# Kernel tuning notes

Measured on AMD Instinct MI355X. Metric: run time of the kernel, lower is better.

Reference implementation:

```python
import jax, jax.numpy as jnp
import numpy as np

NEG_INIT = -1.0e9


def setup_inputs() -> dict:
    key = jax.random.key(0)
    k1, k2, k3, k4, k5, k6, k7 = jax.random.split(key, 7)
    N, D, d_att, G = 262144, 512, 128, 512
    feats = jax.random.normal(k1, (N, D), dtype=jnp.float32)
    index = jnp.sort(jax.random.randint(k2, (N,), 0, G, dtype=jnp.int64))
    # torch Linear params: weight (out,in), bias (out,)
    Vw = jax.random.normal(k3, (d_att, D), dtype=jnp.float32) / np.sqrt(D)
    Vb = jax.random.normal(k4, (d_att,), dtype=jnp.float32) * 0.01
    Uw = jax.random.normal(k5, (d_att, D), dtype=jnp.float32) / np.sqrt(D)
    Ub = jax.random.normal(k6, (d_att,), dtype=jnp.float32) * 0.01
    ww = jax.random.normal(k7, (1, d_att), dtype=jnp.float32) / np.sqrt(d_att)
    return {"feats": feats, "index": index, "num_groups": G,
            "Vw": Vw, "Vb": Vb, "Uw": Uw, "Ub": Ub, "ww": ww}


def reference(feats, index, num_groups, Vw, Vb, Uw, Ub, ww):
    # gated attention MLP: A = tanh(V x) * sigmoid(U x); scores = w A
    A = jnp.tanh(feats @ Vw.T + Vb) * jax.nn.sigmoid(feats @ Uw.T + Ub)  # (N, d_att)
    scores = (A @ ww.T)[:, 0]  # (N,)
    # segment max with -1e9 init (matches scatter_reduce amax include_self)
    max_per_group = jax.ops.segment_max(scores, index, num_segments=num_groups)
    max_per_group = jnp.maximum(max_per_group, NEG_INIT)  # empty segments -> -1e9
    exp_scores = jnp.exp(scores - max_per_group[index])
    denom = jax.ops.segment_sum(exp_scores, index, num_segments=num_groups)
    weights = exp_scores / (denom[index] + 1e-8)
    # weighted scatter-sum pooling: (num_groups, D)
    out = jax.ops.segment_sum(feats * weights[:, None], index, num_segments=num_groups)
    return out
```

## Files before the change

kernel.cpp:

```cpp
#include <hip/hip_runtime.h>
#include <hip/hip_fp8.h>
#include <cstddef>

#define NEG_INIT -1.0e9f

typedef _Float16 f16x8 __attribute__((ext_vector_type(8)));
typedef _Float16 f16x4 __attribute__((ext_vector_type(4)));
typedef float f32x4 __attribute__((ext_vector_type(4)));

constexpr int D   = 512;
constexpr int BM  = 32;
constexpr int BK  = 32;
constexpr int NKS = D / BK;
constexpr int LDH = 520;
constexpr int LDR = 528;
constexpr int PS  = 516;
constexpr float RSC  = 2048.f;
constexpr float RISC = 1.f / 2048.f;

__global__ __launch_bounds__(64) void k_wprep(const float* __restrict__ Vw,
                                              const float* __restrict__ Uw,
                                              _Float16* __restrict__ Wfrag) {
    const int bid  = blockIdx.x;
    const int lane = threadIdx.x;
    const int j    = bid & 3;
    const int ks   = (bid >> 2) & 15;
    const int wc   = bid >> 6;
    const int l15  = lane & 15;
    const int kgrp = lane >> 4;
    const float* src = (j < 2 ? Vw + (size_t)(wc * 32 + j * 16 + l15) * D
                              : Uw + (size_t)(wc * 32 + (j - 2) * 16 + l15) * D)
                       + ks * BK + kgrp * 8;
    f16x8 h;
    #pragma unroll
    for (int e = 0; e < 8; ++e) h[e] = (_Float16)src[e];
    *(f16x8*)(Wfrag + ((size_t)bid * 64 + lane) * 8) = h;
}

__global__ __launch_bounds__(256) void k_bounds(const int* __restrict__ index,
                                                int N, int G,
                                                int* __restrict__ start) {
    int g = blockIdx.x * blockDim.x + threadIdx.x;
    if (g > G) return;
    int lo = 0, hi = N;
    while (lo < hi) {
        int mid = (lo + hi) >> 1;
        if (index[mid] < g) lo = mid + 1; else hi = mid;
    }
    start[g] = lo;
}

__global__ __launch_bounds__(512, 6) void k_fused(
    const float* __restrict__ feats, const _Float16* __restrict__ Wfrag,
    const float* __restrict__ Vb, const float* __restrict__ Ub,
    const float* __restrict__ ww, const int* __restrict__ index,
    const int* __restrict__ start, float* __restrict__ P, int N)
{
    __shared__ __align__(16) _Float16 Xh[BM][LDH];
    __shared__ __align__(4)  unsigned char Xr8[BM * LDR];
    __shared__ float sred[8][BM];
    __shared__ float srow[BM];
    __shared__ float evals[BM];

    const int t    = threadIdx.x;
    const int lane = t & 63;
    const int wc   = t >> 6;
    const int l15  = lane & 15;
    const int kgrp = lane >> 4;
    const int blk  = blockIdx.x;
    const int rb   = blk * BM;

    {
        const int xrow = t >> 4;
        const int xcb  = t & 15;
        const float* xg = feats + (size_t)min(rb + xrow, N - 1) * D + xcb * 4;
        #pragma unroll
        for (int k = 0; k < 8; ++k) {
            f32x4 v = *(const f32x4*)(xg + k * 64);
            f16x4 h;
            unsigned int rp = 0;
            #pragma unroll
            for (int e = 0; e < 4; ++e) {
                h[e] = (_Float16)v[e];
                float res = (v[e] - (float)h[e]) * RSC;
                __hip_fp8_e4m3 q(res);
                rp |= (unsigned int)q.__x << (8 * e);
            }
            *(f16x4*)&Xh[xrow][k * 64 + xcb * 4] = h;
            *(unsigned int*)&Xr8[xrow * LDR + k * 64 + xcb * 4] = rp;
        }
    }
    __syncthreads();

    const _Float16* wbV = Wfrag + (size_t)(wc >> 1) * 32768
                                + (size_t)(wc & 1) * 512 + (size_t)lane * 8;
    const _Float16* wbU = wbV + 1024;

    f32x4 accV[2], accU[2];
    #pragma unroll
    for (int i = 0; i < 2; ++i) {
        accV[i] = (f32x4){0.f, 0.f, 0.f, 0.f};
        accU[i] = (f32x4){0.f, 0.f, 0.f, 0.f};
    }

    #pragma unroll 4
    for (int ks = 0; ks < NKS; ++ks) {
        f16x8 bv = *(const f16x8*)(wbV + (size_t)ks * 2048);
        f16x8 bu = *(const f16x8*)(wbU + (size_t)ks * 2048);
        f16x8 ha[2];
        #pragma unroll
        for (int i = 0; i < 2; ++i)
            ha[i] = *(const f16x8*)&Xh[i * 16 + l15][ks * BK + kgrp * 8];
        #pragma unroll
        for (int i = 0; i < 2; ++i) {
            accV[i] = __builtin_amdgcn_mfma_f32_16x16x32_f16(ha[i], bv, accV[i], 0, 0, 0);
            accU[i] = __builtin_amdgcn_mfma_f32_16x16x32_f16(ha[i], bu, accU[i], 0, 0, 0);
        }
    }

    {
        const int c = wc * 16 + l15;
        const float vb = Vb[c], ub = Ub[c], w = ww[c];
        float part[2][4];
        #pragma unroll
        for (int i = 0; i < 2; ++i)
            #pragma unroll
            for (int r = 0; r < 4; ++r) {
                float v = accV[i][r] + vb;
                float u = accU[i][r] + ub;
                part[i][r] = w * tanhf(v) * (1.f / (1.f + expf(-u)));
            }
        #pragma unroll
        for (int off = 1; off < 16; off <<= 1)
            #pragma unroll
            for (int i = 0; i < 2; ++i)
                #pragma unroll
                for (int r = 0; r < 4; ++r)
                    part[i][r] += __shfl_xor(part[i][r], off);
        if (l15 == 0) {
            #pragma unroll
            for (int i = 0; i < 2; ++i)
                #pragma unroll
                for (int r = 0; r < 4; ++r)
                    sred[wc][i * 16 + kgrp * 4 + r] = part[i][r];
        }
    }
    __syncthreads();
    if (t < BM) {
        float s = sred[0][t];
        #pragma unroll
        for (int w8 = 1; w8 < 8; ++w8) s += sred[w8][t];
        srow[t] = s;
    }
    __syncthreads();

    const int gl = index[rb];
    const int gh = index[rb + BM - 1];
    for (int g = gl + wc; g <= gh; g += 8) {
        const int r0 = max(start[g], rb), r1 = min(start[g + 1], rb + BM);
        if (r1 <= r0) continue;
        const bool in = (lane >= r0 - rb) && (lane < r1 - rb);
        float m = in ? srow[lane] : NEG_INIT;
        #pragma unroll
        for (int off = 32; off; off >>= 1) m = fmaxf(m, __shfl_xor(m, off));
        float e = in ? expf(srow[lane] - m) : 0.f;
        if (in) evals[lane] = e;
        float s = e;
        #pragma unroll
        for (int off = 32; off; off >>= 1) s += __shfl_xor(s, off);
        if (lane == 0) {
            float* slot = P + (size_t)(blk + g) * PS;
            slot[0] = m; slot[1] = s;
        }
    }
    __syncthreads();

    for (int g = gl; g <= gh; ++g) {
        const int r0 = max(start[g], rb), r1 = min(start[g + 1], rb + BM);
        if (r1 <= r0) continue;
        float a = 0.f;
        for (int r = r0; r < r1; ++r) {
            const int rr = r - rb;
            float h = (float)Xh[rr][t];
            __hip_fp8_e4m3 q;
            q.__x = Xr8[rr * LDR + t];
            float x = fmaf((float)q, RISC, h);
            a = fmaf(evals[rr], x, a);
        }
        P[(size_t)(blk + g) * PS + 4 + t] = a;
    }
}

__global__ __launch_bounds__(512) void k_merge(const float* __restrict__ P,
                                               const int* __restrict__ start,
                                               float* __restrict__ out)
{
    const int g = blockIdx.x, t = threadIdx.x;
    const int s0 = start[g], s1 = start[g + 1];
    if (s0 >= s1) { out[(size_t)g * D + t] = 0.f; return; }
    const int b0 = s0 >> 5, b1 = (s1 - 1) >> 5;
    float M = NEG_INIT;
    for (int b = b0; b <= b1; ++b)
        M = fmaxf(M, P[(size_t)(b + g) * PS]);
    float den = 0.f, acc = 0.f;
    for (int b = b0; b <= b1; ++b) {
        const float* slot = P + (size_t)(b + g) * PS;
        float w = expf(slot[0] - M);
        den += w * slot[1];
        acc += w * slot[4 + t];
    }
    out[(size_t)g * D + t] = acc / (den + 1e-8f);
}

extern "C" void kernel_launch(void* const* d_in, const int* in_sizes, int n_in,
                              void* d_out, int out_size, void* d_ws, size_t ws_size,
                              hipStream_t stream) {
    const float* feats = (const float*)d_in[0];
    const int*   index = (const int*)d_in[1];
    const float* Vw = (const float*)d_in[3];
    const float* Vb = (const float*)d_in[4];
    const float* Uw = (const float*)d_in[5];
    const float* Ub = (const float*)d_in[6];
    const float* ww = (const float*)d_in[7];
    float* out = (float*)d_out;

    const int N = in_sizes[1];
    const int G = out_size / D;
    const int nblk = (N + BM - 1) / BM;

    _Float16* Wfrag = (_Float16*)d_ws;
    int* start      = (int*)(Wfrag + (size_t)256 * 512);
    size_t off      = (size_t)256 * 512 * 2 + (G + 1) * 4;
    off             = (off + 15) & ~(size_t)15;
    float* P        = (float*)((char*)d_ws + off);

    hipLaunchKernelGGL(k_wprep, dim3(256), dim3(64), 0, stream, Vw, Uw, Wfrag);
    hipLaunchKernelGGL(k_bounds, dim3((G + 1 + 255) / 256), dim3(256), 0, stream,
                       index, N, G, start);
    hipLaunchKernelGGL(k_fused, dim3(nblk), dim3(512), 0, stream,
                       feats, Wfrag, Vb, Ub, ww, index, start, P, N);
    hipLaunchKernelGGL(k_merge, dim3(G), dim3(512), 0, stream, P, start, out);
}
```

Baseline: 239.3 us.

## Make fused kernel persistent over tiles with register-prefetched feature loads

Each block now processes 16 consecutive 32-row tiles instead of one, prefetching the next tile's feature rows into registers while the current tile's MFMA, softmax and pooling run. The aim is to hide global-load latency behind compute and amortize block setup. This cuts the grid size 16x and holds 32 extra float registers per thread, so the occupancy hint drops from 6 to 4. It also adds a barrier per tile.

```diff
diff --git a/kernel.cpp b/kernel.cpp
--- a/kernel.cpp
+++ b/kernel.cpp
@@ -12,6 +12,7 @@
 constexpr int BM  = 32;
 constexpr int BK  = 32;
 constexpr int NKS = D / BK;
+constexpr int TPB = 16;
 constexpr int LDH = 520;
 constexpr int LDR = 528;
 constexpr int PS  = 516;
@@ -50,7 +51,7 @@
     start[g] = lo;
 }
 
-__global__ __launch_bounds__(512, 6) void k_fused(
+__global__ __launch_bounds__(512, 4) void k_fused(
     const float* __restrict__ feats, const _Float16* __restrict__ Wfrag,
     const float* __restrict__ Vb, const float* __restrict__ Ub,
     const float* __restrict__ ww, const int* __restrict__ index,
@@ -67,127 +68,153 @@
     const int wc   = t >> 6;
     const int l15  = lane & 15;
     const int kgrp = lane >> 4;
-    const int blk  = blockIdx.x;
-    const int rb   = blk * BM;
-
-    {
-        const int xrow = t >> 4;
-        const int xcb  = t & 15;
-        const float* xg = feats + (size_t)min(rb + xrow, N - 1) * D + xcb * 4;
+
+    const int nTiles    = (N + BM - 1) / BM;
+    const int tile_base = blockIdx.x * TPB;
+    const int tile_end  = min(tile_base + TPB, nTiles);
+    if (tile_base >= nTiles) return;
+
+    const int xrow = t >> 4;
+    const int xcb  = t & 15;
+
+    float4 xa[8];
+    auto issueX = [&](int tile) {
+        const float* xg = feats + (size_t)min(tile * BM + xrow, N - 1) * D + xcb * 4;
+        #pragma unroll
+        for (int k = 0; k < 8; ++k)
+            xa[k] = *(const float4*)(xg + k * 64);
+    };
+    auto commitX = [&]() {
         #pragma unroll
         for (int k = 0; k < 8; ++k) {
-            f32x4 v = *(const f32x4*)(xg + k * 64);
+            float4 v = xa[k];
             f16x4 h;
             unsigned int rp = 0;
             #pragma unroll
             for (int e = 0; e < 4; ++e) {
-                h[e] = (_Float16)v[e];
-                float res = (v[e] - (float)h[e]) * RSC;
+                float ve = (&v.x)[e];
+                h[e] = (_Float16)ve;
+                float res = (ve - (float)h[e]) * RSC;
                 __hip_fp8_e4m3 q(res);
                 rp |= (unsigned int)q.__x << (8 * e);
             }
             *(f16x4*)&Xh[xrow][k * 64 + xcb * 4] = h;
             *(unsigned int*)&Xr8[xrow * LDR + k * 64 + xcb * 4] = rp;
         }
-    }
-    __syncthreads();
+    };
 
     const _Float16* wbV = Wfrag + (size_t)(wc >> 1) * 32768
                                 + (size_t)(wc & 1) * 512 + (size_t)lane * 8;
     const _Float16* wbU = wbV + 1024;
 
-    f32x4 accV[2], accU[2];
-    #pragma unroll
-    for (int i = 0; i < 2; ++i) {
-        accV[i] = (f32x4){0.f, 0.f, 0.f, 0.f};
-        accU[i] = (f32x4){0.f, 0.f, 0.f, 0.f};
-    }
-
-    #pragma unroll 4
-    for (int ks = 0; ks < NKS; ++ks) {
-        f16x8 bv = *(const f16x8*)(wbV + (size_t)ks * 2048);
-        f16x8 bu = *(const f16x8*)(wbU + (size_t)ks * 2048);
-        f16x8 ha[2];
-        #pragma unroll
-        for (int i = 0; i < 2; ++i)
-            ha[i] = *(const f16x8*)&Xh[i * 16 + l15][ks * BK + kgrp * 8];
+    issueX(tile_base);
+    commitX();
+    if (tile_base + 1 < tile_end) issueX(tile_base + 1);
+    __syncthreads();
+
+    for (int it = 0; it < TPB && tile_base + it < nTiles; ++it) {
+        const int tile = tile_base + it;
+        const int rb   = tile * BM;
+
+        f32x4 accV[2], accU[2];
         #pragma unroll
         for (int i = 0; i < 2; ++i) {
-            accV[i] = __builtin_amdgcn_mfma_f32_16x16x32_f16(ha[i], bv, accV[i], 0, 0, 0);
-            accU[i] = __builtin_amdgcn_mfma_f32_16x16x32_f16(ha[i], bu, accU[i], 0, 0, 0);
-        }
-    }
-
-    {
-        const int c = wc * 16 + l15;
-        const float vb = Vb[c], ub = Ub[c], w = ww[c];
-        float part[2][4];
-        #pragma unroll
-        for (int i = 0; i < 2; ++i)
-            #pragma unroll
-            for (int r = 0; r < 4; ++r) {
-                float v = accV[i][r] + vb;
-                float u = accU[i][r] + ub;
-                part[i][r] = w * tanhf(v) * (1.f / (1.f + expf(-u)));
-            }
-        #pragma unroll
-        for (int off = 1; off < 16; off <<= 1)
+            accV[i] = (f32x4){0.f, 0.f, 0.f, 0.f};
+            accU[i] = (f32x4){0.f, 0.f, 0.f, 0.f};
+        }
+        #pragma unroll 4
+        for (int ks = 0; ks < NKS; ++ks) {
+            f16x8 bv = *(const f16x8*)(wbV + (size_t)ks * 2048);
+            f16x8 bu = *(const f16x8*)(wbU + (size_t)ks * 2048);
+            f16x8 ha[2];
+            #pragma unroll
+            for (int i = 0; i < 2; ++i)
+                ha[i] = *(const f16x8*)&Xh[i * 16 + l15][ks * BK + kgrp * 8];
+            #pragma unroll
+            for (int i = 0; i < 2; ++i) {
+                accV[i] = __builtin_amdgcn_mfma_f32_16x16x32_f16(ha[i], bv, accV[i], 0, 0, 0);
+                accU[i] = __builtin_amdgcn_mfma_f32_16x16x32_f16(ha[i], bu, accU[i], 0, 0, 0);
+            }
+        }
+
+        {
+            const int c = wc * 16 + l15;
+            const float vb = Vb[c], ub = Ub[c], w = ww[c];
+            float part[2][4];
             #pragma unroll
             for (int i = 0; i < 2; ++i)
                 #pragma unroll
-                for (int r = 0; r < 4; ++r)
-                    part[i][r] += __shfl_xor(part[i][r], off);
-        if (l15 == 0) {
-            #pragma unroll
-            for (int i = 0; i < 2; ++i)
+                for (int r = 0; r < 4; ++r) {
+                    float v = accV[i][r] + vb;
+                    float u = accU[i][r] + ub;
+                    part[i][r] = w * tanhf(v) * (1.f / (1.f + expf(-u)));
+                }
+            #pragma unroll
+            for (int off = 1; off < 16; off <<= 1)
                 #pragma unroll
-                for (int r = 0; r < 4; ++r)
-                    sred[wc][i * 16 + kgrp * 4 + r] = part[i][r];
-        }
-    }
-    __syncthreads();
-    if (t < BM) {
-        float s = sred[0][t];
-        #pragma unroll
-        for (int w8 = 1; w8 < 8; ++w8) s += sred[w8][t];
-        srow[t] = s;
-    }
-    __syncthreads();
-
-    const int gl = index[rb];
-    const int gh = index[rb + BM - 1];
-    for (int g = gl + wc; g <= gh; g += 8) {
-        const int r0 = max(start[g], rb), r1 = min(start[g + 1], rb + BM);
-        if (r1 <= r0) continue;
-        const bool in = (lane >= r0 - rb) && (lane < r1 - rb);
-        float m = in ? srow[lane] : NEG_INIT;
-        #pragma unroll
-        for (int off = 32; off; off >>= 1) m = fmaxf(m, __shfl_xor(m, off));
-        float e = in ? expf(srow[lane] - m) : 0.f;
-        if (in) evals[lane] = e;
-        float s = e;
-        #pragma unroll
-        for (int off = 32; off; off >>= 1) s += __shfl_xor(s, off);
-        if (lane == 0) {
-            float* slot = P + (size_t)(blk + g) * PS;
-            slot[0] = m; slot[1] = s;
-        }
-    }
-    __syncthreads();
-
-    for (int g = gl; g <= gh; ++g) {
-        const int r0 = max(start[g], rb), r1 = min(start[g + 1], rb + BM);
-        if (r1 <= r0) continue;
-        float a = 0.f;
-        for (int r = r0; r < r1; ++r) {
-            const int rr = r - rb;
-            float h = (float)Xh[rr][t];
-            __hip_fp8_e4m3 q;
-            q.__x = Xr8[rr * LDR + t];
-            float x = fmaf((float)q, RISC, h);
-            a = fmaf(evals[rr], x, a);
-        }
-        P[(size_t)(blk + g) * PS + 4 + t] = a;
+                for (int i = 0; i < 2; ++i)
+                    #pragma unroll
+                    for (int r = 0; r < 4; ++r)
+                        part[i][r] += __shfl_xor(part[i][r], off);
+            if (l15 == 0) {
+                #pragma unroll
+                for (int i = 0; i < 2; ++i)
+                    #pragma unroll
+                    for (int r = 0; r < 4; ++r)
+                        sred[wc][i * 16 + kgrp * 4 + r] = part[i][r];
+            }
+        }
+        __syncthreads();
+        if (t < BM) {
+            float s = sred[0][t];
+            #pragma unroll
+            for (int w8 = 1; w8 < 8; ++w8) s += sred[w8][t];
+            srow[t] = s;
+        }
+        __syncthreads();
+
+        const int gl = index[rb];
+        const int gh = index[min(rb + BM - 1, N - 1)];
+        for (int g = gl + wc; g <= gh; g += 8) {
+            const int r0 = max(start[g], rb), r1 = min(start[g + 1], rb + BM);
+            if (r1 <= r0) continue;
+            const bool in = (lane >= r0 - rb) && (lane < r1 - rb);
+            float m = in ? srow[lane] : NEG_INIT;
+            #pragma unroll
+            for (int off = 32; off; off >>= 1) m = fmaxf(m, __shfl_xor(m, off));
+            float e = in ? expf(srow[lane] - m) : 0.f;
+            if (in) evals[lane] = e;
+            float s = e;
+            #pragma unroll
+            for (int off = 32; off; off >>= 1) s += __shfl_xor(s, off);
+            if (lane == 0) {
+                float* slot = P + (size_t)(tile + g) * PS;
+                slot[0] = m; slot[1] = s;
+            }
+        }
+        __syncthreads();
+
+        for (int g = gl; g <= gh; ++g) {
+            const int r0 = max(start[g], rb), r1 = min(start[g + 1], rb + BM);
+            if (r1 <= r0) continue;
+            float a = 0.f;
+            for (int r = r0; r < r1; ++r) {
+                const int rr = r - rb;
+                float h = (float)Xh[rr][t];
+                __hip_fp8_e4m3 q;
+                q.__x = Xr8[rr * LDR + t];
+                float x = fmaf((float)q, RISC, h);
+                a = fmaf(evals[rr], x, a);
+            }
+            P[(size_t)(tile + g) * PS + 4 + t] = a;
+        }
+        __syncthreads();
+
+        if (it + 1 < TPB && tile + 1 < nTiles) {
+            commitX();
+            if (it + 2 < TPB && tile + 2 < nTiles) issueX(tile + 2);
+            __syncthreads();
+        }
     }
 }
 
@@ -226,7 +253,8 @@
 
     const int N = in_sizes[1];
     const int G = out_size / D;
-    const int nblk = (N + BM - 1) / BM;
+    const int nTiles = (N + BM - 1) / BM;
+    const int nblk   = (nTiles + TPB - 1) / TPB;
 
     _Float16* Wfrag = (_Float16*)d_ws;
     int* start      = (int*)(Wfrag + (size_t)256 * 512);
```

After: 259.4 us. 8.4% more time.
